# Kernel optimization log

Measured on AMD Instinct MI355X. Metric: run time of the kernel, lower is better.

## Reference

```python
import jax, jax.numpy as jnp
import numpy as np

E = 1024      # embed_dim (== embed_dim_)
NH = 8        # num_heads
HD = E // NH  # head_dim
BS1 = 2048
BS2 = 2048
EPS = 1e-5


def _layernorm(x, g, b):
    m = jnp.mean(x, axis=-1, keepdims=True)
    v = jnp.mean(jnp.square(x - m), axis=-1, keepdims=True)
    return (x - m) * jax.lax.rsqrt(v + EPS) * g + b


def setup_inputs() -> dict:
    key = jax.random.key(0)
    ks = jax.random.split(key, 16)
    s = 1.0 / np.sqrt(E)
    s4 = 1.0 / np.sqrt(4 * E)
    inp = {
        "x1": jax.random.normal(ks[0], (BS1, E), jnp.float32),
        "x2": jax.random.normal(ks[1], (BS2, E), jnp.float32),
        "Wq": jax.random.uniform(ks[2], (E, E), jnp.float32, -s, s),
        "bq": jax.random.uniform(ks[3], (E,), jnp.float32, -s, s),
        "Wk": jax.random.uniform(ks[4], (E, E), jnp.float32, -s, s),
        "bk": jax.random.uniform(ks[5], (E,), jnp.float32, -s, s),
        "Wv": jax.random.uniform(ks[6], (E, E), jnp.float32, -s, s),
        "bv": jax.random.uniform(ks[7], (E,), jnp.float32, -s, s),
        "Wo": jax.random.uniform(ks[8], (E, E), jnp.float32, -s, s),
        "bo": jax.random.uniform(ks[9], (E,), jnp.float32, -s, s),
        "W1": jax.random.uniform(ks[10], (4 * E, E), jnp.float32, -s, s),
        "b1": jax.random.uniform(ks[11], (4 * E,), jnp.float32, -s, s),
        "W2": jax.random.uniform(ks[12], (E, 4 * E), jnp.float32, -s4, s4),
        "b2": jax.random.uniform(ks[13], (E,), jnp.float32, -s4, s4),
        "g1": jnp.ones((E,), jnp.float32),
        "be1": jnp.zeros((E,), jnp.float32),
        "g2": jnp.ones((E,), jnp.float32),
        "be2": jnp.zeros((E,), jnp.float32),
    }
    return inp


def reference(x1, x2, Wq, bq, Wk, bk, Wv, bv, Wo, bo, W1, b1, W2, b2, g1, be1, g2, be2):
    scale = HD ** -0.5
    # Projections; attention runs over the batch axis (n=bs1, m=bs2)
    q = (x1 @ Wq.T + bq).reshape(BS1, NH, HD)   # [n,h,d]
    k = (x2 @ Wk.T + bk).reshape(BS2, NH, HD)   # [m,h,d]
    v = (x2 @ Wv.T + bv).reshape(BS2, NH, HD)   # [m,h,d]
    scores = jnp.einsum('nhd,mhd->nmh', q, k) * scale  # [n,m,h]
    # NOTE: faithful to source: softmax over the HEADS axis (dim=-1)
    probs = jax.nn.softmax(scores, axis=-1)
    # dropout is identity in eval mode
    attn = jnp.einsum('nmh,mhd->nhd', probs, v).reshape(BS1, E)
    attn = attn @ Wo.T + bo
    h = _layernorm(x1 + attn, g1, be1)
    ffn = jax.nn.relu(h @ W1.T + b1) @ W2.T + b2
    return _layernorm(h + ffn, g2, be2)
```

## Files before the change

kernel.cpp:

```cpp
#include <hip/hip_runtime.h>

#define BS 2048
#define EMB 1024
#define NHEAD 8
#define HDIM 128

typedef unsigned short u16;
typedef __attribute__((ext_vector_type(8))) short bf16x8;
typedef __attribute__((ext_vector_type(4))) float f32x4;

__device__ __forceinline__ u16 f32_bf16(float f) {
  unsigned u = __float_as_uint(f);
  u += 0x7fffu + ((u >> 16) & 1u);
  return (u16)(u >> 16);
}
__device__ __forceinline__ float bf2f(u16 x) {
  return __uint_as_float((unsigned)x << 16);
}

__device__ __forceinline__ void gld_lds16(const void* g, void* l) {
  __builtin_amdgcn_global_load_lds(
      (const __attribute__((address_space(1))) void*)g,
      (__attribute__((address_space(3))) void*)l, 16, 0, 0);
}

struct CvtArgs { const float* src[8]; };
__global__ __launch_bounds__(256) void cvt_all(CvtArgs a, u16* __restrict__ dst) {
  long i = (long)blockIdx.x * 256 + threadIdx.x;
  int seg = (int)(i >> 18);
  const float* src; long b;
  if (seg < 2)       { src = a.src[0]; b = 0; }
  else if (seg < 4)  { src = a.src[1]; b = 2L << 18; }
  else if (seg == 4) { src = a.src[2]; b = 4L << 18; }
  else if (seg == 5) { src = a.src[3]; b = 5L << 18; }
  else if (seg == 6) { src = a.src[4]; b = 6L << 18; }
  else if (seg == 7) { src = a.src[5]; b = 7L << 18; }
  else if (seg < 12) { src = a.src[6]; b = 8L << 18; }
  else               { src = a.src[7]; b = 12L << 18; }
  float4 v = ((const float4*)src)[i - b];
  ushort4 o;
  o.x = f32_bf16(v.x); o.y = f32_bf16(v.y); o.z = f32_bf16(v.z); o.w = f32_bf16(v.w);
  ((ushort4*)dst)[i] = o;
}

__device__ __forceinline__ void gemm_core(
    const u16* __restrict__ A, const u16* __restrict__ B, void* __restrict__ Cp,
    const float* __restrict__ bias, int K, int lda, int ldb, int ldc,
    long cbase, int mode, int relu, int m0, int n0) {
  __shared__ __align__(16) u16 As[128 * 32];
  __shared__ __align__(16) u16 Bs[128 * 32];
  const int t = threadIdx.x;
  const int lane = t & 63, l15 = lane & 15, quad = lane >> 4;
  const int wv = t >> 6, wr = wv & 1, wc = wv >> 1;
  const int wbase = t & ~63;

  f32x4 acc[4][4];
#pragma unroll
  for (int r = 0; r < 4; ++r)
#pragma unroll
    for (int c = 0; c < 4; ++c) acc[r][c] = (f32x4){0.f, 0.f, 0.f, 0.f};

  for (int k0 = 0; k0 < K; k0 += 32) {
#pragma unroll
    for (int i = 0; i < 2; ++i) {
      int s = i * 256 + t;
      gld_lds16(A + (long)(m0 + (s >> 2)) * lda + k0 + (s & 3) * 8,
                As + (i * 256 + wbase) * 8);
    }
#pragma unroll
    for (int i = 0; i < 2; ++i) {
      int s = i * 256 + t;
      gld_lds16(B + (long)(n0 + (s >> 2)) * ldb + k0 + (s & 3) * 8,
                Bs + (i * 256 + wbase) * 8);
    }
    __syncthreads();
    bf16x8 fa[4], fb[4];
#pragma unroll
    for (int r = 0; r < 4; ++r)
      fa[r] = *(const bf16x8*)&As[(wr * 64 + r * 16 + l15) * 32 + quad * 8];
#pragma unroll
    for (int c = 0; c < 4; ++c)
      fb[c] = *(const bf16x8*)&Bs[(wc * 64 + c * 16 + l15) * 32 + quad * 8];
#pragma unroll
    for (int r = 0; r < 4; ++r)
#pragma unroll
      for (int c = 0; c < 4; ++c)
        acc[r][c] = __builtin_amdgcn_mfma_f32_16x16x32_bf16(fa[r], fb[c], acc[r][c], 0, 0, 0);
    __syncthreads();
  }

#pragma unroll
  for (int r = 0; r < 4; ++r)
#pragma unroll
    for (int c = 0; c < 4; ++c) {
      const int m = m0 + wr * 64 + r * 16 + quad * 4;
      const int n = n0 + wc * 64 + c * 16 + l15;
      const float bv = bias ? bias[n] : 0.f;
      f32x4 v = acc[r][c];
      if (mode == 2) {
        ushort4 o;
        o.x = f32_bf16(v[0] + bv);
        o.y = f32_bf16(v[1] + bv);
        o.z = f32_bf16(v[2] + bv);
        o.w = f32_bf16(v[3] + bv);
        *(ushort4*)((u16*)Cp + cbase + (long)n * ldc + m) = o;
      } else {
#pragma unroll
        for (int i = 0; i < 4; ++i) {
          float x = v[i] + bv;
          if (relu) x = fmaxf(x, 0.f);
          if (mode == 0)
            ((float*)Cp)[cbase + (long)(m + i) * ldc + n] = x;
          else
            ((u16*)Cp)[cbase + (long)(m + i) * ldc + n] = f32_bf16(x);
        }
      }
    }
}

__global__ __launch_bounds__(256) void gemm_bt_k(
    const u16* __restrict__ A, const u16* __restrict__ B, void* __restrict__ C,
    const float* __restrict__ bias, int K, int lda, int ldb, int ldc,
    long aOffZ, long bOffZ, long cOffZ, int mode, int relu) {
  gemm_core(A + (long)blockIdx.z * aOffZ, B + (long)blockIdx.z * bOffZ, C, bias,
            K, lda, ldb, ldc, (long)blockIdx.z * cOffZ, mode, relu,
            blockIdx.y * 128, blockIdx.x * 128);
}

__global__ __launch_bounds__(256) void qkv_kernel(
    const u16* __restrict__ x1b, const u16* __restrict__ x2b,
    const u16* __restrict__ Wqb, const u16* __restrict__ Wkb, const u16* __restrict__ Wvb,
    const float* __restrict__ bq, const float* __restrict__ bk, const float* __restrict__ bv,
    u16* __restrict__ Qb, u16* __restrict__ Kb, u16* __restrict__ Vt) {
  const int z = blockIdx.z;
  const u16* A = (z == 0) ? x1b : x2b;
  const u16* B = (z == 0) ? Wqb : (z == 1) ? Wkb : Wvb;
  void* C = (z == 0) ? (void*)Qb : (z == 1) ? (void*)Kb : (void*)Vt;
  const float* bias = (z == 0) ? bq : (z == 1) ? bk : bv;
  const int mode = (z == 2) ? 2 : 1;
  const int ldc = (z == 2) ? 2048 : 1024;
  gemm_core(A, B, C, bias, 1024, 1024, 1024, ldc, 0, mode, 0,
            blockIdx.y * 128, blockIdx.x * 128);
}

__global__ __launch_bounds__(256, 1) void fused_attn(
    const u16* __restrict__ Qg, const u16* __restrict__ Kg,
    const u16* __restrict__ Vt, u16* __restrict__ parts) {
  __shared__ __align__(16) u16 Qs[2][4096];
  __shared__ __align__(16) u16 Ks[2][16384];
  __shared__ __align__(16) u16 Vs[2][16384];
  __shared__ __align__(16) u16 Ps[4096];
  const int t = threadIdx.x;
  const int lane = t & 63, l15 = lane & 15, quad = lane >> 4;
  const int wv = t >> 6, wbase = t & ~63;
  const int chunk = blockIdx.x;
  const int n0 = blockIdx.y * 32;

  auto stageQ = [&](int h, int b) {
#pragma unroll
    for (int i = 0; i < 2; ++i) {
      int s = i * 256 + t;
      gld_lds16(Qg + (long)(n0 + ((s >> 2) & 31)) * EMB + h * HDIM + (s >> 7) * 32 + (s & 3) * 8,
                &Qs[b][(i * 256 + wbase) * 8]);
    }
  };
  auto stageK = [&](int h, int b, int m0) {
#pragma unroll
    for (int i = 0; i < 8; ++i) {
      int s = i * 256 + t;
      gld_lds16(Kg + (long)(m0 + ((s >> 2) & 127)) * EMB + h * HDIM + (s >> 9) * 32 + (s & 3) * 8,
                &Ks[b][(i * 256 + wbase) * 8]);
    }
  };
  auto stageV = [&](int h, int b, int m0) {
#pragma unroll
    for (int i = 0; i < 8; ++i) {
      int s = i * 256 + t;
      gld_lds16(Vt + (long)(h * HDIM + ((s >> 2) & 127)) * 2048 + m0 + (s >> 9) * 32 + (s & 3) * 8,
                &Vs[b][(i * 256 + wbase) * 8]);
    }
  };

  f32x4 O[8][2][2];
#pragma unroll
  for (int h = 0; h < 8; ++h)
#pragma unroll
    for (int r = 0; r < 2; ++r)
#pragma unroll
      for (int c = 0; c < 2; ++c) O[h][r][c] = (f32x4){0.f, 0.f, 0.f, 0.f};

  stageQ(0, 0);
  stageK(0, 0, chunk * 512);

  for (int mt = 0; mt < 4; ++mt) {
    const int m0 = chunk * 512 + mt * 128;
    f32x4 acc[8][2][2];
#pragma unroll
    for (int h = 0; h < 8; ++h)
#pragma unroll
      for (int r = 0; r < 2; ++r)
#pragma unroll
        for (int c = 0; c < 2; ++c) acc[h][r][c] = (f32x4){0.f, 0.f, 0.f, 0.f};

#pragma unroll
    for (int h = 0; h < 8; ++h) {
      __syncthreads();
      if (h < 7) { stageQ(h + 1, (h + 1) & 1); stageK(h + 1, (h + 1) & 1, m0); }
      const u16* qb = Qs[h & 1];
      const u16* kb = Ks[h & 1];
#pragma unroll
      for (int kk = 0; kk < 4; ++kk) {
        bf16x8 fa[2], fb[2];
#pragma unroll
        for (int r = 0; r < 2; ++r)
          fa[r] = *(const bf16x8*)&qb[kk * 1024 + (r * 16 + l15) * 32 + quad * 8];
#pragma unroll
        for (int c = 0; c < 2; ++c)
          fb[c] = *(const bf16x8*)&kb[kk * 4096 + (wv * 32 + c * 16 + l15) * 32 + quad * 8];
#pragma unroll
        for (int r = 0; r < 2; ++r)
#pragma unroll
          for (int c = 0; c < 2; ++c)
            acc[h][r][c] = __builtin_amdgcn_mfma_f32_16x16x32_bf16(fa[r], fb[c], acc[h][r][c], 0, 0, 0);
      }
    }

    stageV(0, 0, m0);

    const float scale = 0.08838834764831845f;
#pragma unroll
    for (int r = 0; r < 2; ++r)
#pragma unroll
      for (int c = 0; c < 2; ++c)
#pragma unroll
        for (int i = 0; i < 4; ++i) {
          float mx = acc[0][r][c][i];
#pragma unroll
          for (int h = 1; h < 8; ++h) mx = fmaxf(mx, acc[h][r][c][i]);
          float sum = 0.f;
#pragma unroll
          for (int h = 0; h < 8; ++h) {
            float e = __expf((acc[h][r][c][i] - mx) * scale);
            acc[h][r][c][i] = e;
            sum += e;
          }
          float inv = 1.f / sum;
#pragma unroll
          for (int h = 0; h < 8; ++h) acc[h][r][c][i] *= inv;
        }

#pragma unroll
    for (int h = 0; h < 8; ++h) {
      __syncthreads();
#pragma unroll
      for (int r = 0; r < 2; ++r)
#pragma unroll
        for (int c = 0; c < 2; ++c)
#pragma unroll
          for (int i = 0; i < 4; ++i) {
            int n = r * 16 + quad * 4 + i;
            int e = (c * 16 + l15) ^ (quad << 3);
            Ps[wv * 1024 + n * 32 + e] = f32_bf16(acc[h][r][c][i]);
          }
      __syncthreads();
      if (h < 7) stageV(h + 1, (h + 1) & 1, m0);
      if (h == 0 && mt < 3) { stageQ(0, 0); stageK(0, 0, m0 + 128); }
      const u16* vb = Vs[h & 1];
#pragma unroll
      for (int kk = 0; kk < 4; ++kk) {
        bf16x8 fa[2], fb[2];
#pragma unroll
        for (int rr = 0; rr < 2; ++rr)
          fa[rr] = *(const bf16x8*)&Ps[kk * 1024 + (rr * 16 + l15) * 32 +
                                       (((quad ^ (l15 >> 2)) & 3) << 3)];
#pragma unroll
        for (int c = 0; c < 2; ++c)
          fb[c] = *(const bf16x8*)&vb[kk * 4096 + (wv * 32 + c * 16 + l15) * 32 + quad * 8];
#pragma unroll
        for (int rr = 0; rr < 2; ++rr)
#pragma unroll
          for (int c = 0; c < 2; ++c)
            O[h][rr][c] = __builtin_amdgcn_mfma_f32_16x16x32_bf16(fa[rr], fb[c], O[h][rr][c], 0, 0, 0);
      }
    }
  }

#pragma unroll
  for (int h = 0; h < 8; ++h)
#pragma unroll
    for (int r = 0; r < 2; ++r)
#pragma unroll
      for (int c = 0; c < 2; ++c)
#pragma unroll
        for (int i = 0; i < 4; ++i) {
          int n = n0 + r * 16 + quad * 4 + i;
          int col = h * HDIM + wv * 32 + c * 16 + l15;
          parts[(long)chunk * BS * EMB + (long)n * EMB + col] = f32_bf16(O[h][r][c][i]);
        }
}

__global__ __launch_bounds__(256) void reduce4_bf16(
    const u16* __restrict__ p, u16* __restrict__ out) {
  long i = (long)blockIdx.x * 256 + threadIdx.x;
  const long S = (long)BS * EMB / 4;
  ushort4 a0 = ((const ushort4*)p)[i];
  ushort4 a1 = ((const ushort4*)p)[i + S];
  ushort4 a2 = ((const ushort4*)p)[i + 2 * S];
  ushort4 a3 = ((const ushort4*)p)[i + 3 * S];
  ushort4 o;
  o.x = f32_bf16(bf2f(a0.x) + bf2f(a1.x) + bf2f(a2.x) + bf2f(a3.x));
  o.y = f32_bf16(bf2f(a0.y) + bf2f(a1.y) + bf2f(a2.y) + bf2f(a3.y));
  o.z = f32_bf16(bf2f(a0.z) + bf2f(a1.z) + bf2f(a2.z) + bf2f(a3.z));
  o.w = f32_bf16(bf2f(a0.w) + bf2f(a1.w) + bf2f(a2.w) + bf2f(a3.w));
  ((ushort4*)out)[i] = o;
}

__global__ __launch_bounds__(256) void ln_residual3(
    const float* __restrict__ x, const float* __restrict__ y0, const float* __restrict__ y1,
    const float* __restrict__ colb, const float* __restrict__ g, const float* __restrict__ b,
    float* __restrict__ out32, u16* __restrict__ out16) {
  const int row = blockIdx.x, t = threadIdx.x;
  float4 v = ((const float4*)(x + (long)row * EMB))[t];
  float4 u0 = ((const float4*)(y0 + (long)row * EMB))[t];
  float4 u1 = ((const float4*)(y1 + (long)row * EMB))[t];
  float4 cb = ((const float4*)colb)[t];
  v.x += u0.x + u1.x + cb.x;
  v.y += u0.y + u1.y + cb.y;
  v.z += u0.z + u1.z + cb.z;
  v.w += u0.w + u1.w + cb.w;
  float s = v.x + v.y + v.z + v.w;
  float q = v.x * v.x + v.y * v.y + v.z * v.z + v.w * v.w;
#pragma unroll
  for (int off = 32; off > 0; off >>= 1) {
    s += __shfl_xor(s, off);
    q += __shfl_xor(q, off);
  }
  __shared__ float red[8];
  const int wv = t >> 6, lane = t & 63;
  if (lane == 0) { red[wv] = s; red[4 + wv] = q; }
  __syncthreads();
  s = red[0] + red[1] + red[2] + red[3];
  q = red[4] + red[5] + red[6] + red[7];
  const float mean = s * (1.f / EMB);
  const float var = q * (1.f / EMB) - mean * mean;
  const float rstd = rsqrtf(var + 1e-5f);
  float4 gg = ((const float4*)g)[t];
  float4 bb = ((const float4*)b)[t];
  float4 o;
  o.x = (v.x - mean) * rstd * gg.x + bb.x;
  o.y = (v.y - mean) * rstd * gg.y + bb.y;
  o.z = (v.z - mean) * rstd * gg.z + bb.z;
  o.w = (v.w - mean) * rstd * gg.w + bb.w;
  ((float4*)(out32 + (long)row * EMB))[t] = o;
  if (out16) {
    ushort4 ho;
    ho.x = f32_bf16(o.x); ho.y = f32_bf16(o.y); ho.z = f32_bf16(o.z); ho.w = f32_bf16(o.w);
    ((ushort4*)(out16 + (long)row * EMB))[t] = ho;
  }
}

extern "C" void kernel_launch(void* const* d_in, const int* in_sizes, int n_in,
                              void* d_out, int out_size, void* d_ws, size_t ws_size,
                              hipStream_t stream) {
  const float* x1 = (const float*)d_in[0];
  const float* x2 = (const float*)d_in[1];
  const float* Wq = (const float*)d_in[2];
  const float* bq = (const float*)d_in[3];
  const float* Wk = (const float*)d_in[4];
  const float* bk = (const float*)d_in[5];
  const float* Wv = (const float*)d_in[6];
  const float* bv = (const float*)d_in[7];
  const float* Wo = (const float*)d_in[8];
  const float* bo = (const float*)d_in[9];
  const float* W1 = (const float*)d_in[10];
  const float* b1 = (const float*)d_in[11];
  const float* W2 = (const float*)d_in[12];
  const float* b2 = (const float*)d_in[13];
  const float* g1 = (const float*)d_in[14];
  const float* be1 = (const float*)d_in[15];
  const float* g2 = (const float*)d_in[16];
  const float* be2 = (const float*)d_in[17];

  char* ws = (char*)d_ws;
  const size_t MB = 1ull << 20;
  u16* x1b = (u16*)(ws + 0 * MB);
  u16* x2b = (u16*)(ws + 4 * MB);
  u16* Wqb = (u16*)(ws + 8 * MB);
  u16* Wkb = (u16*)(ws + 10 * MB);
  u16* Wvb = (u16*)(ws + 12 * MB);
  u16* Wob = (u16*)(ws + 14 * MB);
  u16* W1b = (u16*)(ws + 16 * MB);
  u16* W2b = (u16*)(ws + 24 * MB);
  u16* Qb  = (u16*)(ws + 32 * MB);
  u16* Kb  = (u16*)(ws + 36 * MB);
  u16* Vtb = (u16*)(ws + 40 * MB);
  u16* attnb = (u16*)(ws + 44 * MB);
  u16* Oparts = (u16*)(ws + 48 * MB);
  float* woP0 = (float*)(ws + 64 * MB);
  float* woP1 = (float*)(ws + 72 * MB);
  float* h32  = (float*)(ws + 80 * MB);
  u16*  h16   = (u16*)(ws + 88 * MB);
  u16*  ffn1b = (u16*)(ws + 92 * MB);
  float* f2P0 = woP0;
  float* f2P1 = woP1;

  CvtArgs ca;
  ca.src[0] = x1; ca.src[1] = x2; ca.src[2] = Wq; ca.src[3] = Wk;
  ca.src[4] = Wv; ca.src[5] = Wo; ca.src[6] = W1; ca.src[7] = W2;
  cvt_all<<<16384, 256, 0, stream>>>(ca, (u16*)ws);

  qkv_kernel<<<dim3(8, 16, 3), 256, 0, stream>>>(x1b, x2b, Wqb, Wkb, Wvb, bq, bk, bv, Qb, Kb, Vtb);

  fused_attn<<<dim3(4, 64), 256, 0, stream>>>(Qb, Kb, Vtb, Oparts);

  reduce4_bf16<<<2048, 256, 0, stream>>>(Oparts, attnb);

  gemm_bt_k<<<dim3(8, 16, 2), 256, 0, stream>>>(attnb, Wob, woP0, nullptr,
                                                512, 1024, 1024, 1024,
                                                512, 512, (long)BS * 1024, 0, 0);

  ln_residual3<<<2048, 256, 0, stream>>>(x1, woP0, woP1, bo, g1, be1, h32, h16);

  gemm_bt_k<<<dim3(32, 16, 1), 256, 0, stream>>>(h16, W1b, ffn1b, b1,
                                                 1024, 1024, 1024, 4096,
                                                 0, 0, 0, 1, 1);

  gemm_bt_k<<<dim3(8, 16, 2), 256, 0, stream>>>(ffn1b, W2b, f2P0, nullptr,
                                                2048, 4096, 4096, 1024,
                                                2048, 2048, (long)BS * 1024, 0, 0);

  ln_residual3<<<2048, 256, 0, stream>>>(h32, f2P0, f2P1, b2, g2, be2, (float*)d_out, nullptr);
}
```

Baseline: 366.5 us.

## Rewrite attention kernel with 16-row tiles and direct global K/V fragment loads

Replaces the 32-row attention block, which double-buffered Q, K and V through LDS, with a 16-row block. The new block loads all of Q into padded LDS once, then reads K and V MFMA operands straight from global memory into registers, with the MFMA operands swapped so the outputs come out transposed. The grid grows from 256 to 512 blocks with less LDS and fewer registers per block, aiming at higher occupancy and fewer barriers. In exchange, K and V are reread from global/L2 by many more blocks, and the per-lane global loads are strided.

```diff
diff --git a/kernel.cpp b/kernel.cpp
--- a/kernel.cpp
+++ b/kernel.cpp
@@ -143,160 +143,125 @@
             blockIdx.y * 128, blockIdx.x * 128);
 }
 
-__global__ __launch_bounds__(256, 1) void fused_attn(
+__global__ __launch_bounds__(256) void fused_attn2(
     const u16* __restrict__ Qg, const u16* __restrict__ Kg,
     const u16* __restrict__ Vt, u16* __restrict__ parts) {
-  __shared__ __align__(16) u16 Qs[2][4096];
-  __shared__ __align__(16) u16 Ks[2][16384];
-  __shared__ __align__(16) u16 Vs[2][16384];
-  __shared__ __align__(16) u16 Ps[4096];
+  __shared__ __align__(16) u16 Qs[16 * 1032];
+  __shared__ __align__(16) u16 Ps[8 * 16 * 136];
   const int t = threadIdx.x;
   const int lane = t & 63, l15 = lane & 15, quad = lane >> 4;
-  const int wv = t >> 6, wbase = t & ~63;
-  const int chunk = blockIdx.x;
-  const int n0 = blockIdx.y * 32;
-
-  auto stageQ = [&](int h, int b) {
-#pragma unroll
-    for (int i = 0; i < 2; ++i) {
-      int s = i * 256 + t;
-      gld_lds16(Qg + (long)(n0 + ((s >> 2) & 31)) * EMB + h * HDIM + (s >> 7) * 32 + (s & 3) * 8,
-                &Qs[b][(i * 256 + wbase) * 8]);
-    }
-  };
-  auto stageK = [&](int h, int b, int m0) {
-#pragma unroll
-    for (int i = 0; i < 8; ++i) {
-      int s = i * 256 + t;
-      gld_lds16(Kg + (long)(m0 + ((s >> 2) & 127)) * EMB + h * HDIM + (s >> 9) * 32 + (s & 3) * 8,
-                &Ks[b][(i * 256 + wbase) * 8]);
-    }
-  };
-  auto stageV = [&](int h, int b, int m0) {
-#pragma unroll
-    for (int i = 0; i < 8; ++i) {
-      int s = i * 256 + t;
-      gld_lds16(Vt + (long)(h * HDIM + ((s >> 2) & 127)) * 2048 + m0 + (s >> 9) * 32 + (s & 3) * 8,
-                &Vs[b][(i * 256 + wbase) * 8]);
-    }
-  };
-
-  f32x4 O[8][2][2];
+  const int wv = t >> 6;
+  const int n0 = blockIdx.x * 16;
+  const int chunk = blockIdx.y;
+
+#pragma unroll
+  for (int it = 0; it < 8; ++it) {
+    int c = it * 256 + t;
+    int n = c >> 7, o = (c & 127) * 8;
+    *(uint4*)&Qs[n * 1032 + o] = *(const uint4*)&Qg[(long)(n0 + n) * 1024 + o];
+  }
+  __syncthreads();
+
+  f32x4 O[8][2];
 #pragma unroll
   for (int h = 0; h < 8; ++h)
 #pragma unroll
-    for (int r = 0; r < 2; ++r)
-#pragma unroll
-      for (int c = 0; c < 2; ++c) O[h][r][c] = (f32x4){0.f, 0.f, 0.f, 0.f};
-
-  stageQ(0, 0);
-  stageK(0, 0, chunk * 512);
-
-  for (int mt = 0; mt < 4; ++mt) {
-    const int m0 = chunk * 512 + mt * 128;
-    f32x4 acc[8][2][2];
+    for (int d = 0; d < 2; ++d) O[h][d] = (f32x4){0.f, 0.f, 0.f, 0.f};
+
+  const float scale = 0.08838834764831845f;
+
+  for (int g = 0; g < 4; ++g) {
+    const int m0 = chunk * 512 + g * 128;
+
+    f32x4 acc[8][2];
 #pragma unroll
     for (int h = 0; h < 8; ++h)
 #pragma unroll
-      for (int r = 0; r < 2; ++r)
-#pragma unroll
-        for (int c = 0; c < 2; ++c) acc[h][r][c] = (f32x4){0.f, 0.f, 0.f, 0.f};
-
+      for (int tt = 0; tt < 2; ++tt) acc[h][tt] = (f32x4){0.f, 0.f, 0.f, 0.f};
+
+    const u16* Kb0 = Kg + (long)(m0 + wv * 32 + l15) * 1024;
+    const u16* Kb1 = Kb0 + 16 * 1024;
 #pragma unroll
     for (int h = 0; h < 8; ++h) {
-      __syncthreads();
-      if (h < 7) { stageQ(h + 1, (h + 1) & 1); stageK(h + 1, (h + 1) & 1, m0); }
-      const u16* qb = Qs[h & 1];
-      const u16* kb = Ks[h & 1];
+      bf16x8 ka[2][4];
 #pragma unroll
       for (int kk = 0; kk < 4; ++kk) {
-        bf16x8 fa[2], fb[2];
-#pragma unroll
-        for (int r = 0; r < 2; ++r)
-          fa[r] = *(const bf16x8*)&qb[kk * 1024 + (r * 16 + l15) * 32 + quad * 8];
-#pragma unroll
-        for (int c = 0; c < 2; ++c)
-          fb[c] = *(const bf16x8*)&kb[kk * 4096 + (wv * 32 + c * 16 + l15) * 32 + quad * 8];
-#pragma unroll
-        for (int r = 0; r < 2; ++r)
-#pragma unroll
-          for (int c = 0; c < 2; ++c)
-            acc[h][r][c] = __builtin_amdgcn_mfma_f32_16x16x32_bf16(fa[r], fb[c], acc[h][r][c], 0, 0, 0);
-      }
-    }
-
-    stageV(0, 0, m0);
-
-    const float scale = 0.08838834764831845f;
-#pragma unroll
-    for (int r = 0; r < 2; ++r)
-#pragma unroll
-      for (int c = 0; c < 2; ++c)
-#pragma unroll
-        for (int i = 0; i < 4; ++i) {
-          float mx = acc[0][r][c][i];
-#pragma unroll
-          for (int h = 1; h < 8; ++h) mx = fmaxf(mx, acc[h][r][c][i]);
-          float sum = 0.f;
-#pragma unroll
-          for (int h = 0; h < 8; ++h) {
-            float e = __expf((acc[h][r][c][i] - mx) * scale);
-            acc[h][r][c][i] = e;
-            sum += e;
-          }
-          float inv = 1.f / sum;
-#pragma unroll
-          for (int h = 0; h < 8; ++h) acc[h][r][c][i] *= inv;
+        ka[0][kk] = *(const bf16x8*)&Kb0[h * 128 + kk * 32 + quad * 8];
+        ka[1][kk] = *(const bf16x8*)&Kb1[h * 128 + kk * 32 + quad * 8];
+      }
+#pragma unroll
+      for (int kk = 0; kk < 4; ++kk) {
+        bf16x8 qb = *(const bf16x8*)&Qs[l15 * 1032 + h * 128 + kk * 32 + quad * 8];
+        acc[h][0] = __builtin_amdgcn_mfma_f32_16x16x32_bf16(ka[0][kk], qb, acc[h][0], 0, 0, 0);
+        acc[h][1] = __builtin_amdgcn_mfma_f32_16x16x32_bf16(ka[1][kk], qb, acc[h][1], 0, 0, 0);
+      }
+    }
+
+#pragma unroll
+    for (int tt = 0; tt < 2; ++tt)
+#pragma unroll
+      for (int i = 0; i < 4; ++i) {
+        float mx = acc[0][tt][i];
+#pragma unroll
+        for (int h = 1; h < 8; ++h) mx = fmaxf(mx, acc[h][tt][i]);
+        float sum = 0.f;
+#pragma unroll
+        for (int h = 0; h < 8; ++h) {
+          float e = __expf((acc[h][tt][i] - mx) * scale);
+          acc[h][tt][i] = e;
+          sum += e;
         }
-
+        float inv = 1.f / sum;
+#pragma unroll
+        for (int h = 0; h < 8; ++h) acc[h][tt][i] *= inv;
+      }
+
+    __syncthreads();
+
+#pragma unroll
+    for (int h = 0; h < 8; ++h)
+#pragma unroll
+      for (int tt = 0; tt < 2; ++tt) {
+        ushort4 o4;
+        o4.x = f32_bf16(acc[h][tt][0]);
+        o4.y = f32_bf16(acc[h][tt][1]);
+        o4.z = f32_bf16(acc[h][tt][2]);
+        o4.w = f32_bf16(acc[h][tt][3]);
+        *(ushort4*)&Ps[(h * 16 + l15) * 136 + wv * 32 + tt * 16 + quad * 4] = o4;
+      }
+    __syncthreads();
+
+    const u16* Vb0 = Vt + (long)(wv * 32 + l15) * 2048 + m0;
+    const u16* Vb1 = Vb0 + 16 * 2048;
 #pragma unroll
     for (int h = 0; h < 8; ++h) {
-      __syncthreads();
-#pragma unroll
-      for (int r = 0; r < 2; ++r)
-#pragma unroll
-        for (int c = 0; c < 2; ++c)
-#pragma unroll
-          for (int i = 0; i < 4; ++i) {
-            int n = r * 16 + quad * 4 + i;
-            int e = (c * 16 + l15) ^ (quad << 3);
-            Ps[wv * 1024 + n * 32 + e] = f32_bf16(acc[h][r][c][i]);
-          }
-      __syncthreads();
-      if (h < 7) stageV(h + 1, (h + 1) & 1, m0);
-      if (h == 0 && mt < 3) { stageQ(0, 0); stageK(0, 0, m0 + 128); }
-      const u16* vb = Vs[h & 1];
+      bf16x8 va[2][4];
 #pragma unroll
       for (int kk = 0; kk < 4; ++kk) {
-        bf16x8 fa[2], fb[2];
-#pragma unroll
-        for (int rr = 0; rr < 2; ++rr)
-          fa[rr] = *(const bf16x8*)&Ps[kk * 1024 + (rr * 16 + l15) * 32 +
-                                       (((quad ^ (l15 >> 2)) & 3) << 3)];
-#pragma unroll
-        for (int c = 0; c < 2; ++c)
-          fb[c] = *(const bf16x8*)&vb[kk * 4096 + (wv * 32 + c * 16 + l15) * 32 + quad * 8];
-#pragma unroll
-        for (int rr = 0; rr < 2; ++rr)
-#pragma unroll
-          for (int c = 0; c < 2; ++c)
-            O[h][rr][c] = __builtin_amdgcn_mfma_f32_16x16x32_bf16(fa[rr], fb[c], O[h][rr][c], 0, 0, 0);
-      }
-    }
-  }
-
+        va[0][kk] = *(const bf16x8*)&Vb0[(long)h * 128 * 2048 + kk * 32 + quad * 8];
+        va[1][kk] = *(const bf16x8*)&Vb1[(long)h * 128 * 2048 + kk * 32 + quad * 8];
+      }
+#pragma unroll
+      for (int kk = 0; kk < 4; ++kk) {
+        bf16x8 pb = *(const bf16x8*)&Ps[(h * 16 + l15) * 136 + kk * 32 + quad * 8];
+        O[h][0] = __builtin_amdgcn_mfma_f32_16x16x32_bf16(va[0][kk], pb, O[h][0], 0, 0, 0);
+        O[h][1] = __builtin_amdgcn_mfma_f32_16x16x32_bf16(va[1][kk], pb, O[h][1], 0, 0, 0);
+      }
+    }
+  }
+
+  u16* pbase = parts + (long)chunk * BS * EMB + (long)(n0 + l15) * EMB;
 #pragma unroll
   for (int h = 0; h < 8; ++h)
 #pragma unroll
-    for (int r = 0; r < 2; ++r)
-#pragma unroll
-      for (int c = 0; c < 2; ++c)
-#pragma unroll
-        for (int i = 0; i < 4; ++i) {
-          int n = n0 + r * 16 + quad * 4 + i;
-          int col = h * HDIM + wv * 32 + c * 16 + l15;
-          parts[(long)chunk * BS * EMB + (long)n * EMB + col] = f32_bf16(O[h][r][c][i]);
-        }
+    for (int dt = 0; dt < 2; ++dt) {
+      ushort4 o4;
+      o4.x = f32_bf16(O[h][dt][0]);
+      o4.y = f32_bf16(O[h][dt][1]);
+      o4.z = f32_bf16(O[h][dt][2]);
+      o4.w = f32_bf16(O[h][dt][3]);
+      *(ushort4*)&pbase[h * 128 + wv * 32 + dt * 16 + quad * 4] = o4;
+    }
 }
 
 __global__ __launch_bounds__(256) void reduce4_bf16(
@@ -411,7 +376,7 @@
 
   qkv_kernel<<<dim3(8, 16, 3), 256, 0, stream>>>(x1b, x2b, Wqb, Wkb, Wvb, bq, bk, bv, Qb, Kb, Vtb);
 
-  fused_attn<<<dim3(4, 64), 256, 0, stream>>>(Qb, Kb, Vtb, Oparts);
+  fused_attn2<<<dim3(128, 4), 256, 0, stream>>>(Qb, Kb, Vtb, Oparts);
 
   reduce4_bf16<<<2048, 256, 0, stream>>>(Oparts, attnb);
 
```

Measured after the change: 414.1 us. 13.0% more time.
